# Kernel optimization log

Measured on AMD Instinct MI355X. Metric: run time of the kernel, lower is better.

Reference implementation:

```python
import jax, jax.numpy as jnp
from jax import lax
import numpy as np

KS = 8        # window size
SS = 4        # shift size = KS // 2
HEADS = 4


def _l2n(t, axis):
    # torch F.normalize: x / clamp(||x||_2, min=eps)
    return t / jnp.maximum(jnp.linalg.norm(t, axis=axis, keepdims=True), 1e-12)


def _to_windows(t, heads, ks):
    # 'b (head c) (h kh) (w kw) -> b head (h w) (kh kw) c'
    b, hc, H, W = t.shape
    c = hc // heads
    hW, wW = H // ks, W // ks
    t = t.reshape(b, heads, c, hW, ks, wW, ks)
    t = t.transpose(0, 1, 3, 5, 4, 6, 2)  # b,h,hW,wW,kh,kw,c
    return t.reshape(b, heads, hW * wW, ks * ks, c)


def _from_windows(t, hW, wW, ks):
    # 'b head (h w) (kh kw) c -> b (head c) (h kh) (w kw)'
    b, heads, nW, kk, c = t.shape
    t = t.reshape(b, heads, hW, wW, ks, ks, c)
    t = t.transpose(0, 1, 6, 2, 4, 3, 5)  # b,h,c,hW,kh,wW,kw
    return t.reshape(b, heads * c, hW * ks, wW * ks)


def _talk_conv(attn, w, hW, wW):
    # Conv3d(heads->heads, kernel (3,3,1), padding same) over the (hW, wW, K)
    # grid; kernel size 1 on K means an independent 2D conv per K slot, so we
    # fold K into the batch dim and run a single 2D conv.
    b, heads, nW, a1, a2 = attn.shape
    K = a1 * a2
    t = attn.reshape(b, heads, hW, wW, K).transpose(0, 4, 1, 2, 3)
    t = t.reshape(b * K, heads, hW, wW)
    t = lax.conv_general_dilated(t, w, (1, 1), 'SAME',
                                 dimension_numbers=('NCHW', 'OIHW', 'NCHW'))
    t = t.reshape(b, K, heads, hW, wW).transpose(0, 2, 3, 4, 1)
    return t.reshape(b, heads, nW, a1, a2)


def _shift_mask(H, W, ks, ss):
    # Swin-style shifted-window mask; pure numpy constant (shapes are static).
    img = np.zeros((H, W), np.float32)
    cnt = 0
    for hs in (slice(0, -ks), slice(-ks, -ss), slice(-ss, None)):
        for ws in (slice(0, -ks), slice(-ks, -ss), slice(-ss, None)):
            img[hs, ws] = cnt
            cnt += 1
    win = img.reshape(H // ks, ks, W // ks, ks).transpose(0, 2, 1, 3).reshape(-1, ks * ks)
    diff = win[:, None, :] - win[:, :, None]
    return jnp.asarray(np.where(diff != 0, -100.0, 0.0).astype(np.float32))


def _forward(x, w_quz, w_kv, temperature, r_talking, g_talking,
             b_talking_w, l_talking_w, dw_u_w, project_w, project_out_w,
             sca_w, sca_b):
    b, c, H, W = x.shape
    hW, wW = H // KS, W // KS
    quz = jnp.einsum('oc,bchw->bohw', w_quz, x)
    q, u, z = jnp.split(quz, 3, axis=1)
    kv = jnp.einsum('oc,bchw->bohw', w_kv, x)
    k, v = jnp.split(kv, 2, axis=1)
    # shift = True
    q, k, v = (jnp.roll(t, (-SS, -SS), axis=(-1, -2)) for t in (q, k, v))
    q, k, v = (_to_windows(t, HEADS, KS) for t in (q, k, v))  # b,h,nW,kk,c
    qb, ql, qg, qr = jnp.split(q, 4, axis=-1)
    kb, kl, kg, kr = jnp.split(k, 4, axis=-1)
    vb, vl, vg, vr = jnp.split(v, 4, axis=-1)
    qb, kb = _l2n(qb, -1), _l2n(kb, -1)
    ql, kl = _l2n(ql, -2), _l2n(kl, -2)
    qg, kg = _l2n(qg, -3), _l2n(kg, -3)
    qr, kr = _l2n(qr, -3), _l2n(kr, -3)
    # 4 branches (n=window index, i/j=position-in-window, c/d=per-branch chan)
    attn_b = jnp.einsum('bhnic,bhnjc->bhnij', qb, kb) * temperature[0]
    attn_l = jnp.einsum('bhnic,bhnid->bhncd', ql, kl) * temperature[1]
    attn_g = jnp.einsum('bhnic,bhnid->bhicd', qg, kg) * temperature[2]
    attn_r = jnp.einsum('bhnic,bhnjc->bhcij', qr, kr) * temperature[3]
    # talking heads
    attn_b = _talk_conv(attn_b, b_talking_w, hW, wW)
    attn_l = _talk_conv(attn_l, l_talking_w, hW, wW)
    attn_g = jnp.einsum('hklt,bhkcd->btlcd', g_talking, attn_g)
    attn_r = jnp.einsum('hcdt,bhcij->btdij', r_talking, attn_r)
    # shifted-window mask on the brightness branch
    attn_b = attn_b + _shift_mask(H, W, KS, SS)[None, None]
    attn_b, attn_l, attn_g, attn_r = (jax.nn.softmax(t, axis=-1)
                                      for t in (attn_b, attn_l, attn_g, attn_r))
    # outputs, all arranged to (b,h,n,i,c) before un-windowing
    out_b = jnp.einsum('bhnij,bhnjc->bhnic', attn_b, vb)
    out_l = jnp.einsum('bhncd,bhnid->bhnic', attn_l, vl)
    out_g = jnp.einsum('bhicd,bhnid->bhnic', attn_g, vg)
    out_r = jnp.einsum('bhcij,bhnjc->bhnic', attn_r, vr)
    out = jnp.concatenate([_from_windows(t, hW, wW, KS)
                           for t in (out_b, out_l, out_g, out_r)], axis=1)
    out = jnp.roll(out, (SS, SS), axis=(-1, -2))
    # simplified channel attention (global avg pool + 1x1 conv with bias)
    s = jnp.mean(out, axis=(2, 3))
    s = jnp.einsum('oc,bc->bo', sca_w, s) + sca_b
    out = jnp.einsum('oc,bchw->bohw', project_w, out * s[:, :, None, None])
    dw = lax.conv_general_dilated(u, dw_u_w, (1, 1), 'SAME',
                                  feature_group_count=u.shape[1],
                                  dimension_numbers=('NCHW', 'OIHW', 'NCHW'))
    out = out + dw
    return jnp.einsum('oc,bchw->bohw', project_out_w, out * z)


def setup_inputs() -> dict:
    key = jax.random.key(0)
    ks = jax.random.split(key, 12)
    dim, h_dim = 64, 128
    cd = h_dim // HEADS // 4
    b, H, W = 4, 192, 192
    r = lambda i, shp, s: jax.random.normal(ks[i], shp, jnp.float32) * s
    return {
        'x': jax.random.normal(ks[0], (b, dim, H, W), jnp.float32),
        'w_quz': r(1, (3 * h_dim, dim), 0.1),
        'w_kv': r(2, (2 * h_dim, dim), 0.1),
        'temperature': jnp.ones((4, HEADS, 1, 1, 1), jnp.float32),
        'r_talking': r(3, (HEADS, cd, cd, HEADS), 0.2),
        'g_talking': r(4, (HEADS, KS * KS, KS * KS, HEADS), 0.05),
        'b_talking_w': r(5, (HEADS, HEADS, 3, 3), 0.2),
        'l_talking_w': r(6, (HEADS, HEADS, 3, 3), 0.2),
        'dw_u_w': r(7, (h_dim, 1, 3, 3), 0.2),
        'project_w': r(8, (h_dim, h_dim), 0.08),
        'project_out_w': r(9, (dim, h_dim), 0.08),
        'sca_w': r(10, (h_dim, h_dim), 0.08),
        'sca_b': jnp.zeros((h_dim,), jnp.float32),
    }


def reference(x, w_quz, w_kv, temperature, r_talking, g_talking,
              b_talking_w, l_talking_w, dw_u_w, project_w, project_out_w,
              sca_w, sca_b):
    return _forward(x, w_quz, w_kv, temperature, r_talking, g_talking,
                    b_talking_w, l_talking_w, dw_u_w, project_w,
                    project_out_w, sca_w, sca_b)
```

## Files before the change

### kernel.cpp

```cpp
#include <hip/hip_runtime.h>
#include <hip/hip_fp16.h>
#include <cstdint>
#include <cstddef>

#define BB   4
#define CIN  64
#define HD   128
#define NH   4
#define CHW  32
#define CB   8
#define IMG  192
#define SSH  4
#define NWS  24
#define NWIN 576
#define KK   64
#define HWP  (IMG*IMG)

static const size_t NQK16  = (size_t)NH*NWIN*KK*16;
static const size_t NV32   = (size_t)NH*NWIN*KK*CHW;
static const size_t NGR    = (size_t)NH*KK*NWIN*CB;
static const size_t NSP    = (size_t)HD*HWP;
static const size_t NATTNL = (size_t)NH*NWIN*64;
static const size_t NATTNG = (size_t)NH*KK*64;
static const size_t NATTNR = (size_t)NH*CB*KK*KK;
static const size_t NPART  = (size_t)8*NATTNR;

__device__ inline float wave_max(float v){
  #pragma unroll
  for (int s=1;s<64;s<<=1) v = fmaxf(v, __shfl_xor(v, s));
  return v;
}
__device__ inline float wave_sum(float v){
  #pragma unroll
  for (int s=1;s<64;s<<=1) v += __shfl_xor(v, s);
  return v;
}
__device__ inline float g8_max(float v){
  v = fmaxf(v, __shfl_xor(v,1)); v = fmaxf(v, __shfl_xor(v,2)); v = fmaxf(v, __shfl_xor(v,4));
  return v;
}
__device__ inline float g8_sum(float v){
  v += __shfl_xor(v,1); v += __shfl_xor(v,2); v += __shfl_xor(v,4);
  return v;
}
__device__ inline int regionc(int y){ return (y < IMG-8) ? 0 : ((y < IMG-4) ? 1 : 2); }

__device__ inline size_t widx(int h,int n,int i,int c){
  return (((size_t)h*NWIN + n)*KK + i)*CHW + c;
}
__device__ inline size_t widx16(int h,int n,int i,int c){
  return (((size_t)h*NWIN + n)*KK + i)*16 + c;
}
__device__ inline size_t gidx(int h,int i,int n,int c){
  return (((size_t)(h*KK + i))*NWIN + n)*CB + c;
}
__device__ inline size_t ridx(int h,int c,int n,int i){
  return (((size_t)(h*CB + c))*NWIN + n)*KK + i;
}
__device__ inline size_t bidx(int n,int i,int j,int h){
  return ((((size_t)n*KK + i)*KK + j)*NH) + h;
}

__global__ __launch_bounds__(256) void k1_proj(
    const float* __restrict__ x, const float* __restrict__ wquz, const float* __restrict__ wkv,
    float* __restrict__ qw, float* __restrict__ kw, __half* __restrict__ vw,
    float* __restrict__ qg, float* __restrict__ kg,
    float* __restrict__ qr, float* __restrict__ kr,
    float* __restrict__ u, float* __restrict__ zbuf, int bsel)
{
  __shared__ float xs[64][20];
  __shared__ float tb[128][17];
  int blk = blockIdx.x;
  int xc = blk % 12, y = blk / 12;
  int x0 = xc*16;
  int t = threadIdx.x;
  {
    int c = t >> 2, p4 = (t & 3)*4;
    float4 v = *(const float4*)&x[((size_t)(bsel*CIN+c)*IMG + y)*IMG + x0 + p4];
    *(float4*)&xs[c][p4] = v;
  }
  int py  = (y + IMG - SSH) % IMG;
  int kh  = py & 7, hwq = py >> 3;
  int wwA = ((x0 - SSH + IMG) % IMG) >> 3;
  int wwB = x0 >> 3;
  int wwC = (x0 + 8) >> 3;
  int pnA = hwq*NWS + wwA, pnB = hwq*NWS + wwB, pnC = hwq*NWS + wwC;
  int piA = kh*8 + 4, piB = kh*8, piC = kh*8;
  #define PN_(p) ((p)<4 ? pnA : ((p)<12 ? pnB : pnC))
  #define PI_(p) ((p)<4 ? (piA+(p)) : ((p)<12 ? (piB+(p)-4) : (piC+(p)-12)))
  __syncthreads();

  int o;
  if (t < 64)       o = (t>>4)*32 + (t&15);
  else if (t < 96)  o = ((t-64)>>3)*32 + 16 + (t&7);
  else if (t < 128) o = ((t-96)>>3)*32 + 24 + (t&7);
  else              o = t;

  {
    const float* wr = wquz + (size_t)o*CIN;
    float acc[16];
    #pragma unroll
    for (int p = 0; p < 16; ++p) acc[p] = 0.f;
    for (int cc = 0; cc < 64; cc += 4){
      float4 w4 = *(const float4*)(wr + cc);
      #pragma unroll
      for (int p = 0; p < 16; ++p){
        acc[p] += w4.x * xs[cc  ][p];
        acc[p] += w4.y * xs[cc+1][p];
        acc[p] += w4.z * xs[cc+2][p];
        acc[p] += w4.w * xs[cc+3][p];
      }
    }
    if (t < 64){
      int h = t >> 4, c = t & 15;
      #pragma unroll
      for (int p = 0; p < 16; ++p) qw[widx16(h,PN_(p),PI_(p),c)] = acc[p];
    } else if (t < 96){
      int h = (t-64) >> 3, cg = t & 7;
      #pragma unroll
      for (int p = 0; p < 16; ++p) qg[gidx(h,PI_(p),PN_(p),cg)] = acc[p];
    } else if (t < 128){
      int h = (t-96) >> 3, cr = t & 7;
      *(float4*)&qr[ridx(h,cr,pnA,piA)]   = make_float4(acc[0],acc[1],acc[2],acc[3]);
      *(float4*)&qr[ridx(h,cr,pnB,piB)]   = make_float4(acc[4],acc[5],acc[6],acc[7]);
      *(float4*)&qr[ridx(h,cr,pnB,piB+4)] = make_float4(acc[8],acc[9],acc[10],acc[11]);
      *(float4*)&qr[ridx(h,cr,pnC,piC)]   = make_float4(acc[12],acc[13],acc[14],acc[15]);
    } else {
      int ch = o - 128;
      #pragma unroll
      for (int p = 0; p < 16; ++p) tb[ch][p] = acc[p];
    }
  }
  __syncthreads();
  {
    int px = t & 15, chg = t >> 4;
    size_t ub = (size_t)y*IMG + x0 + px;
    #pragma unroll
    for (int cc = 0; cc < 8; ++cc){
      int ch = chg*8 + cc;
      u[(size_t)ch*HWP + ub] = tb[ch][px];
    }
  }

  {
    const float* wr = wkv + (size_t)o*CIN;
    float acc[16];
    #pragma unroll
    for (int p = 0; p < 16; ++p) acc[p] = 0.f;
    for (int cc = 0; cc < 64; cc += 4){
      float4 w4 = *(const float4*)(wr + cc);
      #pragma unroll
      for (int p = 0; p < 16; ++p){
        acc[p] += w4.x * xs[cc  ][p];
        acc[p] += w4.y * xs[cc+1][p];
        acc[p] += w4.z * xs[cc+2][p];
        acc[p] += w4.w * xs[cc+3][p];
      }
    }
    if (t < 64){
      int h = t >> 4, c = t & 15;
      #pragma unroll
      for (int p = 0; p < 16; ++p) kw[widx16(h,PN_(p),PI_(p),c)] = acc[p];
    } else if (t < 96){
      int h = (t-64) >> 3, cg = t & 7;
      #pragma unroll
      for (int p = 0; p < 16; ++p) kg[gidx(h,PI_(p),PN_(p),cg)] = acc[p];
    } else if (t < 128){
      int h = (t-96) >> 3, cr = t & 7;
      *(float4*)&kr[ridx(h,cr,pnA,piA)]   = make_float4(acc[0],acc[1],acc[2],acc[3]);
      *(float4*)&kr[ridx(h,cr,pnB,piB)]   = make_float4(acc[4],acc[5],acc[6],acc[7]);
      *(float4*)&kr[ridx(h,cr,pnB,piB+4)] = make_float4(acc[8],acc[9],acc[10],acc[11]);
      *(float4*)&kr[ridx(h,cr,pnC,piC)]   = make_float4(acc[12],acc[13],acc[14],acc[15]);
    } else {
      int oc = o - 128; int h = oc >> 5, c = oc & 31;
      #pragma unroll
      for (int p = 0; p < 16; ++p) vw[widx(h,PN_(p),PI_(p),c)] = __float2half(acc[p]);
    }
  }

  __syncthreads();
  {
    int zr = t >> 1, ph = t & 1;
    const float* wr = wquz + (size_t)(256 + zr)*CIN;
    int pb = ph*8;
    float acc[8];
    #pragma unroll
    for (int p = 0; p < 8; ++p) acc[p] = 0.f;
    for (int cc = 0; cc < 64; cc += 4){
      float4 w4 = *(const float4*)(wr + cc);
      #pragma unroll
      for (int p = 0; p < 8; ++p){
        acc[p] += w4.x * xs[cc  ][pb+p];
        acc[p] += w4.y * xs[cc+1][pb+p];
        acc[p] += w4.z * xs[cc+2][pb+p];
        acc[p] += w4.w * xs[cc+3][pb+p];
      }
    }
    #pragma unroll
    for (int p = 0; p < 8; ++p) tb[zr][pb+p] = acc[p];
  }
  __syncthreads();
  {
    int px = t & 15, chg = t >> 4;
    size_t zb = (size_t)y*IMG + x0 + px;
    #pragma unroll
    for (int cc = 0; cc < 8; ++cc){
      int ch = chg*8 + cc;
      zbuf[(size_t)ch*HWP + zb] = tb[ch][px];
    }
  }
  #undef PN_
  #undef PI_
}

__global__ __launch_bounds__(256) void kA(
    const float* __restrict__ qw, const float* __restrict__ kw,
    const float* __restrict__ qg, const float* __restrict__ kg,
    const float* __restrict__ qr, const float* __restrict__ kr,
    const float* __restrict__ temp,
    __half* __restrict__ attnB, float* __restrict__ attnL,
    float* __restrict__ attnG, float* __restrict__ part,
    float* __restrict__ invqr, float* __restrict__ invkr)
{
  __shared__ __align__(16) char smem[36864];
  int blk = blockIdx.x;
  int t = threadIdx.x;

  if (blk < 576){
    float (*qs)[64][9] = (float(*)[64][9])smem;
    int j = t >> 2, h = t & 3;
    int n = blk;
    size_t base = widx16(h,n,j,0);
    float q8[CB], k8[CB];
    float sq = 0.f, sk2 = 0.f;
    #pragma unroll
    for (int c = 0; c < CB; ++c){
      q8[c] = qw[base+c]; sq += q8[c]*q8[c];
      k8[c] = kw[base+c]; sk2 += k8[c]*k8[c];
    }
    float invq = 1.f/fmaxf(sqrtf(sq),1e-12f), invk = 1.f/fmaxf(sqrtf(sk2),1e-12f);
    #pragma unroll
    for (int c = 0; c < CB; ++c){ qs[h][j][c] = q8[c]*invq; k8[c] *= invk; }
    __syncthreads();
    float tmp = temp[h];
    __half* ob = attnB + bidx(n,0,0,0);
    for (int i = 0; i < KK; ++i){
      float a = 0.f;
      #pragma unroll
      for (int c = 0; c < CB; ++c) a += qs[h][i][c]*k8[c];
      ob[(size_t)i*256 + t] = __float2half(a * tmp);
    }
  } else if (blk < 1152){
    int b2 = blk - 576;
    float (*qs)[64][8] = (float(*)[64][8])smem;
    float (*ks)[64][8] = (float(*)[64][8])(smem + 8192);
    float (*invqA)[8] = (float(*)[8])(smem + 16384);
    float (*invkA)[8] = (float(*)[8])(smem + 16384 + 128);
    int wv = t >> 6, tl = t & 63;
    int gid = b2*4 + wv;
    int n = gid % NWIN, h = gid / NWIN;
    size_t base = widx16(h,n,tl,8);
    #pragma unroll
    for (int c = 0; c < CB; ++c){ qs[wv][tl][c] = qw[base+c]; ks[wv][tl][c] = kw[base+c]; }
    __syncthreads();
    int c8 = tl & 7, ig = tl >> 3;
    float sq = 0.f, sk2 = 0.f;
    for (int i = ig; i < KK; i += 8){
      float a = qs[wv][i][c8]; sq += a*a;
      float b = ks[wv][i][c8]; sk2 += b*b;
    }
    #pragma unroll
    for (int m = 8; m < 64; m <<= 1){ sq += __shfl_xor(sq,m); sk2 += __shfl_xor(sk2,m); }
    if (tl < 8){ invqA[wv][tl] = 1.f/fmaxf(sqrtf(sq),1e-12f); invkA[wv][tl] = 1.f/fmaxf(sqrtf(sk2),1e-12f); }
    __syncthreads();
    int c = tl >> 3, d = tl & 7;
    float a = 0.f;
    for (int i = 0; i < KK; ++i) a += qs[wv][i][c]*ks[wv][i][d];
    attnL[(size_t)gid*64 + tl] = a * invqA[wv][c] * invkA[wv][d] * temp[NH + h];
  } else if (blk < 1408){
    int b2 = blk - 1152;
    int i = b2 & 63, h = b2 >> 6;
    float* sq = (float*)smem;
    float* sk = sq + 512;
    float (*redA)[64] = (float(*)[64])(smem + 4096);
    float (*redQ)[64] = (float(*)[64])(smem + 4096 + 1024);
    float (*redK)[64] = (float(*)[64])(smem + 4096 + 2048);
    size_t base = ((size_t)(h*KK+i))*NWIN*CB;
    int np = t >> 6, cd = t & 63, c = cd >> 3, d = cd & 7;
    float a = 0.f, qs2 = 0.f, ks2 = 0.f;
    for (int n0 = 0; n0 < NWIN; n0 += 64){
      __syncthreads();
      for (int idx = t; idx < 512; idx += 256){
        sq[idx] = qg[base + (size_t)n0*CB + idx];
        sk[idx] = kg[base + (size_t)n0*CB + idx];
      }
      __syncthreads();
      for (int nn = np; nn < 64; nn += 4){
        float qv = sq[nn*8+c], kv = sk[nn*8+d];
        a += qv*kv; qs2 += qv*qv; ks2 += kv*kv;
      }
    }
    __syncthreads();
    redA[np][cd] = a; redQ[np][cd] = qs2; redK[np][cd] = ks2;
    __syncthreads();
    if (t < 64){
      float at = redA[0][t]+redA[1][t]+redA[2][t]+redA[3][t];
      float qt = redQ[0][t]+redQ[1][t]+redQ[2][t]+redQ[3][t];
      float kt = redK[0][t]+redK[1][t]+redK[2][t]+redK[3][t];
      at *= (1.f/fmaxf(sqrtf(qt),1e-12f)) * (1.f/fmaxf(sqrtf(kt),1e-12f)) * temp[2*NH + h];
      attnG[(size_t)(h*KK+i)*64 + t] = at;
    }
  } else if (blk < 1664){
    int b2 = blk - 1408;
    int chunk = b2 >> 5, hc = b2 & 31;
    int n0 = chunk*72;
    float* sq = (float*)smem;
    float* sk = sq + 72*64;
    size_t base = (size_t)hc*NWIN*KK + (size_t)n0*KK;
    for (int idx = t; idx < 72*64/4; idx += 256){
      *(float4*)&sq[idx*4] = *(const float4*)&qr[base + (size_t)idx*4];
      *(float4*)&sk[idx*4] = *(const float4*)&kr[base + (size_t)idx*4];
    }
    __syncthreads();
    int j = t & 63, ig = t >> 6;
    float acc[16];
    #pragma unroll
    for (int p = 0; p < 16; ++p) acc[p] = 0.f;
    for (int nn = 0; nn < 72; ++nn){
      float kv = sk[nn*64+j];
      #pragma unroll
      for (int p = 0; p < 16; ++p) acc[p] += sq[nn*64 + ig*16 + p]*kv;
    }
    float* ob = part + (size_t)b2*4096;
    #pragma unroll
    for (int p = 0; p < 16; ++p) ob[(size_t)(ig*16+p)*64 + j] = acc[p];
  } else {
    int hc = blk - 1664;
    float (*rq)[64] = (float(*)[64])smem;
    float (*rk)[64] = (float(*)[64])(smem + 1024);
    size_t base = (size_t)hc*NWIN*KK;
    int i = t & 63, ng = t >> 6;
    float sq = 0.f, sk2 = 0.f;
    for (int n = ng; n < NWIN; n += 4){
      float a = qr[base + (size_t)n*KK + i]; sq  += a*a;
      float b = kr[base + (size_t)n*KK + i]; sk2 += b*b;
    }
    rq[ng][i] = sq; rk[ng][i] = sk2;
    __syncthreads();
    if (t < 64){
      float s = rq[0][t]+rq[1][t]+rq[2][t]+rq[3][t];
      invqr[hc*KK + t] = 1.f/fmaxf(sqrtf(s),1e-12f);
    } else if (t < 128){
      int i2 = t - 64;
      float s = rk[0][i2]+rk[1][i2]+rk[2][i2]+rk[3][i2];
      invkr[hc*KK + i2] = 1.f/fmaxf(sqrtf(s),1e-12f);
    }
  }
}

__global__ __launch_bounds__(256) void kB(
    const __half* __restrict__ attnB, const float* __restrict__ btw,
    const __half* __restrict__ vw, float* __restrict__ outa,
    const float* __restrict__ attnL, const float* __restrict__ ltw,
    const float* __restrict__ attnG, const float* __restrict__ gtalk,
    float* __restrict__ attnGp,
    const float* __restrict__ part, const float* __restrict__ invqr,
    const float* __restrict__ invkr, const float* __restrict__ temp,
    float* __restrict__ attnR,
    const float* __restrict__ u, const float* __restrict__ dww,
    float* __restrict__ dwu)
{
  __shared__ __align__(16) char smem[12800];
  int blk = blockIdx.x;
  int t = threadIdx.x;

  if (blk < 9216){
    float (*pbuf)[4][66] = (float(*)[4][66])smem;
    float (*vv)[8][66]   = (float(*)[8][66])(smem + 4224);
    int ig = blk / NWIN, n = blk % NWIN;
    int i0 = ig*4;
    int hw = n / NWS, ww = n % NWS;
    int w = t >> 6, l = t & 63;
    {
      uint4 pk = *(const uint4*)(vw + widx(w, n, l, 0));
      __half2 v01 = *reinterpret_cast<__half2*>(&pk.x);
      __half2 v23 = *reinterpret_cast<__half2*>(&pk.y);
      __half2 v45 = *reinterpret_cast<__half2*>(&pk.z);
      __half2 v67 = *reinterpret_cast<__half2*>(&pk.w);
      float2 f01 = __half22float2(v01), f23 = __half22float2(v23);
      float2 f45 = __half22float2(v45), f67 = __half22float2(v67);
      vv[w][0][l] = f01.x; vv[w][1][l] = f01.y; vv[w][2][l] = f23.x; vv[w][3][l] = f23.y;
      vv[w][4][l] = f45.x; vv[w][5][l] = f45.y; vv[w][6][l] = f67.x; vv[w][7][l] = f67.y;
    }
    int i = i0 + w;
    float a0 = 0.f, a1 = 0.f, a2 = 0.f, a3 = 0.f;
    #pragma unroll
    for (int nb = 0; nb < 9; ++nb){
      const int dy = nb/3 - 1, dx = nb%3 - 1;
      int hw2 = hw + dy, ww2 = ww + dx;
      if (hw2 >= 0 && hw2 < NWS && ww2 >= 0 && ww2 < NWS){
        int n2 = hw2*NWS + ww2;
        const uint2* pb = (const uint2*)(attnB + bidx(n2, i, 0, 0));
        uint2 pk = pb[l];
        __half2 p01 = *reinterpret_cast<__half2*>(&pk.x);
        __half2 p23 = *reinterpret_cast<__half2*>(&pk.y);
        float2 f01 = __half22float2(p01);
        float2 f23 = __half22float2(p23);
        a0 += btw[0*36 + 0*9 + nb]*f01.x + btw[0*36 + 1*9 + nb]*f01.y
            + btw[0*36 + 2*9 + nb]*f23.x + btw[0*36 + 3*9 + nb]*f23.y;
        a1 += btw[1*36 + 0*9 + nb]*f01.x + btw[1*36 + 1*9 + nb]*f01.y
            + btw[1*36 + 2*9 + nb]*f23.x + btw[1*36 + 3*9 + nb]*f23.y;
        a2 += btw[2*36 + 0*9 + nb]*f01.x + btw[2*36 + 1*9 + nb]*f01.y
            + btw[2*36 + 2*9 + nb]*f23.x + btw[2*36 + 3*9 + nb]*f23.y;
        a3 += btw[3*36 + 0*9 + nb]*f01.x + btw[3*36 + 1*9 + nb]*f01.y
            + btw[3*36 + 2*9 + nb]*f23.x + btw[3*36 + 3*9 + nb]*f23.y;
      }
    }
    int kh = i >> 3, kwd = i & 7;
    int cntI = regionc(hw*8 + kh)*3 + regionc(ww*8 + kwd);
    int cntJ = regionc(hw*8 + (l>>3))*3 + regionc(ww*8 + (l&7));
    float mval = (cntI != cntJ) ? -100.f : 0.f;
    a0 += mval; a1 += mval; a2 += mval; a3 += mval;
    {
      float m0 = wave_max(a0); float e0 = __expf(a0 - m0); pbuf[0][w][l] = e0 / wave_sum(e0);
      float m1 = wave_max(a1); float e1 = __expf(a1 - m1); pbuf[1][w][l] = e1 / wave_sum(e1);
      float m2 = wave_max(a2); float e2 = __expf(a2 - m2); pbuf[2][w][l] = e2 / wave_sum(e2);
      float m3 = wave_max(a3); float e3 = __expf(a3 - m3); pbuf[3][w][l] = e3 / wave_sum(e3);
    }
    __syncthreads();
    {
      int i2 = l >> 4, c = (l >> 1) & 7, jq = l & 1;
      const float* pr = &pbuf[w][i2][jq*32];
      const float* vr = &vv[w][c][jq*32];
      float s = 0.f;
      #pragma unroll
      for (int q = 0; q < 32; ++q) s += pr[q] * vr[q];
      s += __shfl_xor(s, 1);
      if (jq == 0){
        int ii = i0 + i2;
        int khh = ii >> 3, kww = ii & 7;
        int Y = (hw*8 + khh + SSH) % IMG;
        int X = (ww*8 + kww + SSH) % IMG;
        outa[((size_t)(w*CB + c)*HWP) + (size_t)Y*IMG + X] = s;
      }
    }
  } else if (blk < 9792){
    int n = blk - 9216;
    int hw = n/NWS, ww = n%NWS;
    float (*rows)[9][64] = (float(*)[9][64])smem;
    float* wt = (float*)(smem + 9216);
    float (*P)[8][8] = (float(*)[8][8])(smem + 9792);
    if (t < NH*NH*9) wt[t] = ltw[t];
    for (int l = t; l < NH*9*64; l += 256){
      int h = l/(9*64); int nb = (l/64)%9; int cd = l & 63;
      int dy = nb/3-1, dx = nb%3-1; int hw2 = hw+dy, ww2 = ww+dx;
      float v = 0.f;
      if (hw2>=0 && hw2<NWS && ww2>=0 && ww2<NWS)
        v = attnL[((size_t)h*NWIN + hw2*NWS + ww2)*64 + cd];
      rows[h][nb][cd] = v;
    }
    __syncthreads();
    int tt = t >> 6; int cd = t & 63; int c = cd >> 3, d = cd & 7;
    float a = 0.f;
    #pragma unroll
    for (int h = 0; h < NH; ++h)
      #pragma unroll
      for (int nb = 0; nb < 9; ++nb)
        a += wt[(tt*NH + h)*9 + nb] * rows[h][nb][cd];
    float m = g8_max(a);
    float e = __expf(a - m);
    P[tt][c][d] = e / g8_sum(e);
    __syncthreads();
    int i = t & 63;
    size_t vbase = widx(tt, n, i, 8);
    float vl[CB];
    #pragma unroll
    for (int d2 = 0; d2 < CB; ++d2) vl[d2] = __half2float(vw[vbase + d2]);
    int kh = i>>3, kwd = i&7;
    int Y = (hw*8+kh+SSH)%IMG, X = (ww*8+kwd+SSH)%IMG;
    #pragma unroll
    for (int c2 = 0; c2 < CB; ++c2){
      float o = 0.f;
      #pragma unroll
      for (int d2 = 0; d2 < CB; ++d2) o += P[tt][c2][d2]*vl[d2];
      outa[((size_t)(32 + tt*CB + c2)*IMG + Y)*IMG + X] = o;
    }
  } else if (blk < 9856){
    int bb = blk - 9792;
    int w = t >> 6, cd = t & 63;
    int idx = bb*4 + w;
    int l = idx & 63, t2 = idx >> 6;
    float a = 0.f;
    for (int h = 0; h < NH; ++h)
      for (int k = 0; k < KK; ++k)
        a += gtalk[((size_t)(h*KK + k)*KK + l)*NH + t2] * attnG[((size_t)h*KK + k)*64 + cd];
    float m = g8_max(a);
    float e = __expf(a - m);
    attnGp[((size_t)t2*KK + l)*64 + cd] = e / g8_sum(e);
  } else if (blk < 10368){
    int e = (blk - 9856)*256 + t;
    float s = 0.f;
    #pragma unroll
    for (int ch = 0; ch < 8; ++ch) s += part[(size_t)ch*NATTNR + e];
    int hc = e >> 12, ij = e & 4095, i = ij >> 6, j = ij & 63;
    attnR[e] = s * invqr[hc*64+i] * invkr[hc*64+j] * temp[3*NH + (hc>>3)];
  } else {
    int bb = blk - 10368;
    int ch = bb / 48; int y0 = (bb % 48) * 4;
    float (*rows)[192] = (float(*)[192])smem;
    for (int idx = t; idx < 6*48; idx += 256){
      int r = idx / 48, px4 = (idx % 48)*4;
      int yy = y0 - 1 + r;
      float4 v = {0.f,0.f,0.f,0.f};
      if (yy >= 0 && yy < IMG) v = *(const float4*)&u[(size_t)ch*HWP + (size_t)yy*IMG + px4];
      rows[r][px4] = v.x; rows[r][px4+1] = v.y; rows[r][px4+2] = v.z; rows[r][px4+3] = v.w;
    }
    float kw9[9];
    #pragma unroll
    for (int q = 0; q < 9; ++q) kw9[q] = dww[ch*9 + q];
    __syncthreads();
    int r = t >> 6, lane = t & 63;
    for (int kx = 0; kx < 3; ++kx){
      int px = lane + kx*64;
      float s = 0.f;
      #pragma unroll
      for (int dy = 0; dy < 3; ++dy){
        #pragma unroll
        for (int dx = -1; dx <= 1; ++dx){
          int xx = px + dx;
          if (xx >= 0 && xx < IMG) s += kw9[dy*3 + dx + 1] * rows[r+dy][xx];
        }
      }
      dwu[(size_t)ch*HWP + (size_t)(y0+r)*IMG + px] = s;
    }
  }
}

__global__ __launch_bounds__(256) void kC(
    const float* __restrict__ attnGp, const __half* __restrict__ vw,
    float* __restrict__ outa,
    const float* __restrict__ attnR, const float* __restrict__ rtalk,
    float* __restrict__ attnRp)
{
  __shared__ __align__(16) char smem[16512];
  int blk = blockIdx.x;
  int t = threadIdx.x;

  if (blk < 2304){
    float* P = (float*)smem;
    int n = blk % NWIN; int t2 = blk / NWIN;
    for (int l = t; l < KK*64; l += 256) P[l] = attnGp[(size_t)t2*KK*64 + l];
    __syncthreads();
    int i = t >> 2; int c0 = (t & 3)*2;
    size_t vbase = widx(t2, n, i, 16);
    float vg[8];
    #pragma unroll
    for (int d = 0; d < 8; ++d) vg[d] = __half2float(vw[vbase + d]);
    int hw = n/NWS, ww = n%NWS; int kh = i>>3, kwd = i&7;
    int Y = (hw*8+kh+SSH)%IMG, X = (ww*8+kwd+SSH)%IMG;
    for (int c = c0; c < c0+2; ++c){
      float o = 0.f;
      #pragma unroll
      for (int d = 0; d < 8; ++d) o += P[(i*8 + c)*8 + d]*vg[d];
      outa[((size_t)(64 + t2*CB + c)*IMG + Y)*IMG + X] = o;
    }
  } else {
    int bb = blk - 2304;
    int d = bb % CB; int t2 = bb / CB;
    float (*S)[64] = (float(*)[64])smem;
    float* wr2 = (float*)(smem + 16384);
    if (t < 32){ int h = t >> 3, c = t & 7; wr2[t] = rtalk[((size_t)(h*CB + c)*CB + d)*NH + t2]; }
    __syncthreads();
    int j = t & 63; int ig = t >> 6;
    float acc[16];
    #pragma unroll
    for (int p = 0; p < 16; ++p) acc[p] = 0.f;
    for (int hc = 0; hc < 32; ++hc){
      float w = wr2[hc];
      const float* Ar = attnR + (size_t)hc*KK*KK;
      #pragma unroll
      for (int p = 0; p < 16; ++p) acc[p] += w * Ar[(size_t)(ig*16+p)*KK + j];
    }
    #pragma unroll
    for (int p = 0; p < 16; ++p) S[ig*16+p][j] = acc[p];
    __syncthreads();
    for (int r = ig; r < 64; r += 4){
      float a = S[r][j];
      float m = wave_max(a);
      float e = __expf(a - m);
      attnRp[(((size_t)t2*CB + d)*KK + r)*KK + j] = e / wave_sum(e);
    }
  }
}

__global__ __launch_bounds__(256) void k7c(
    const float* __restrict__ attnRp, const __half* __restrict__ vw, float* __restrict__ outa)
{
  int n = blockIdx.x % NWIN; int t2 = blockIdx.x / NWIN;
  __shared__ float vr[KK][CB];
  int t = threadIdx.x;
  for (int l = t; l < KK*CB; l += 256){
    int j = l >> 3, c = l & 7;
    vr[j][c] = __half2float(vw[widx(t2, n, j, 24 + c)]);
  }
  __syncthreads();
  int i = t & 63; int cg = t >> 6;
  int hw = n/NWS, ww = n%NWS; int kh = i>>3, kwd = i&7;
  int Y = (hw*8+kh+SSH)%IMG, X = (ww*8+kwd+SSH)%IMG;
  for (int c = cg*2; c < cg*2+2; ++c){
    const float* Pr = attnRp + (((size_t)t2*CB + c)*KK + i)*KK;
    float o = 0.f;
    for (int j = 0; j < KK; ++j) o += Pr[j]*vr[j][c];
    outa[((size_t)(96 + t2*CB + c)*IMG + Y)*IMG + X] = o;
  }
}

__global__ __launch_bounds__(256) void k8_mean(const float* __restrict__ outa, float* __restrict__ meanb){
  int ch = blockIdx.x;
  const float4* p = (const float4*)(outa + (size_t)ch*HWP);
  float s = 0.f;
  for (int l = threadIdx.x; l < HWP/4; l += 256){
    float4 v = p[l]; s += v.x+v.y+v.z+v.w;
  }
  __shared__ float red[256];
  red[threadIdx.x] = s; __syncthreads();
  for (int k = 128; k > 0; k >>= 1){
    if (threadIdx.x < k) red[threadIdx.x] += red[threadIdx.x + k];
    __syncthreads();
  }
  if (threadIdx.x == 0) meanb[ch] = red[0] / (float)HWP;
}

#define PADX 68
__global__ __launch_bounds__(256) void k9a(
    const float* __restrict__ outa, const float* __restrict__ meanb,
    const float* __restrict__ scaw, const float* __restrict__ scab,
    const float* __restrict__ projw, const float* __restrict__ dwu,
    const float* __restrict__ zbuf, float* __restrict__ out2z)
{
  __shared__ float WT[128][128];
  __shared__ float xsv[128][PADX];
  __shared__ float sv[128];
  int t = threadIdx.x;
  if (t < 128){
    float s = scab[t];
    const float* srow = scaw + (size_t)t*HD;
    for (int c = 0; c < HD; c += 4){
      float4 w = *(const float4*)&srow[c];
      float4 mm = *(const float4*)&meanb[c];
      s += w.x*mm.x + w.y*mm.y + w.z*mm.z + w.w*mm.w;
    }
    sv[t] = s;
  }
  for (int idx = t; idx < 4096; idx += 256){
    int o = idx & 127; int c4 = (idx >> 7) * 4;
    float4 w = *(const float4*)&projw[(size_t)o*HD + c4];
    WT[c4][o] = w.x; WT[c4+1][o] = w.y; WT[c4+2][o] = w.z; WT[c4+3][o] = w.w;
  }
  int px4 = (t & 15) * 4; int og8 = (t >> 4) * 8;
  for (int tile = 0; tile < 2; ++tile){
    int tid = blockIdx.x * 2 + tile;
    int y = tid / 3, x0 = (tid % 3) * 64;
    size_t sb = (size_t)y*IMG + x0;
    __syncthreads();
    for (int idx = t; idx < 2048; idx += 256){
      int c = idx >> 4; int p4 = (idx & 15) * 4;
      float4 v = *(const float4*)&outa[(size_t)c*HWP + sb + p4];
      float s = sv[c];
      xsv[c][p4] = v.x*s; xsv[c][p4+1] = v.y*s; xsv[c][p4+2] = v.z*s; xsv[c][p4+3] = v.w*s;
    }
    __syncthreads();
    float acc[8][4];
    #pragma unroll
    for (int a = 0; a < 8; ++a){ acc[a][0]=0.f; acc[a][1]=0.f; acc[a][2]=0.f; acc[a][3]=0.f; }
    for (int c = 0; c < 128; ++c){
      float4 xv = *(const float4*)&xsv[c][px4];
      float4 wA = *(const float4*)&WT[c][og8];
      float4 wB = *(const float4*)&WT[c][og8+4];
      float w8[8] = {wA.x,wA.y,wA.z,wA.w,wB.x,wB.y,wB.z,wB.w};
      #pragma unroll
      for (int a = 0; a < 8; ++a){
        acc[a][0] += w8[a]*xv.x; acc[a][1] += w8[a]*xv.y;
        acc[a][2] += w8[a]*xv.z; acc[a][3] += w8[a]*xv.w;
      }
    }
    #pragma unroll
    for (int oo = 0; oo < 8; ++oo){
      int o = og8 + oo;
      size_t off = (size_t)o*HWP + sb + px4;
      float4 d = *(const float4*)&dwu[off];
      float4 z = *(const float4*)&zbuf[off];
      float4 r;
      r.x = (acc[oo][0]+d.x)*z.x; r.y = (acc[oo][1]+d.y)*z.y;
      r.z = (acc[oo][2]+d.z)*z.z; r.w = (acc[oo][3]+d.w)*z.w;
      *(float4*)&out2z[off] = r;
    }
  }
}

__global__ __launch_bounds__(256) void k9b(
    const float* __restrict__ out2z, const float* __restrict__ projow,
    float* __restrict__ dout, int bsel)
{
  __shared__ float WT2[128][64];
  __shared__ float xsv[128][PADX];
  int t = threadIdx.x;
  for (int idx = t; idx < 2048; idx += 256){
    int o = idx & 63; int c4 = (idx >> 6) * 4;
    float4 w = *(const float4*)&projow[(size_t)o*HD + c4];
    WT2[c4][o] = w.x; WT2[c4+1][o] = w.y; WT2[c4+2][o] = w.z; WT2[c4+3][o] = w.w;
  }
  int px4 = (t & 15) * 4; int og4 = (t >> 4) * 4;
  for (int tile = 0; tile < 2; ++tile){
    int tid = blockIdx.x * 2 + tile;
    int y = tid / 3, x0 = (tid % 3) * 64;
    size_t sb = (size_t)y*IMG + x0;
    __syncthreads();
    for (int idx = t; idx < 2048; idx += 256){
      int c = idx >> 4; int p4 = (idx & 15) * 4;
      float4 v = *(const float4*)&out2z[(size_t)c*HWP + sb + p4];
      xsv[c][p4] = v.x; xsv[c][p4+1] = v.y; xsv[c][p4+2] = v.z; xsv[c][p4+3] = v.w;
    }
    __syncthreads();
    float acc[4][4];
    #pragma unroll
    for (int a = 0; a < 4; ++a){ acc[a][0]=0.f; acc[a][1]=0.f; acc[a][2]=0.f; acc[a][3]=0.f; }
    for (int c = 0; c < 128; ++c){
      float4 xv = *(const float4*)&xsv[c][px4];
      float4 w4 = *(const float4*)&WT2[c][og4];
      float w4a[4] = {w4.x,w4.y,w4.z,w4.w};
      #pragma unroll
      for (int a = 0; a < 4; ++a){
        acc[a][0] += w4a[a]*xv.x; acc[a][1] += w4a[a]*xv.y;
        acc[a][2] += w4a[a]*xv.z; acc[a][3] += w4a[a]*xv.w;
      }
    }
    #pragma unroll
    for (int oo = 0; oo < 4; ++oo){
      int o = og4 + oo;
      float4 r; r.x = acc[oo][0]; r.y = acc[oo][1]; r.z = acc[oo][2]; r.w = acc[oo][3];
      *(float4*)&dout[(size_t)(bsel*CIN + o)*HWP + sb + px4] = r;
    }
  }
}

extern "C" void kernel_launch(void* const* d_in, const int* in_sizes, int n_in,
                              void* d_out, int out_size, void* d_ws, size_t ws_size,
                              hipStream_t stream)
{
  const float* x     = (const float*)d_in[0];
  const float* wquz  = (const float*)d_in[1];
  const float* wkv   = (const float*)d_in[2];
  const float* temp  = (const float*)d_in[3];
  const float* rtalk = (const float*)d_in[4];
  const float* gtalk = (const float*)d_in[5];
  const float* btw   = (const float*)d_in[6];
  const float* ltw   = (const float*)d_in[7];
  const float* dww   = (const float*)d_in[8];
  const float* projw = (const float*)d_in[9];
  const float* projow= (const float*)d_in[10];
  const float* scaw  = (const float*)d_in[11];
  const float* scab  = (const float*)d_in[12];
  float* dout = (float*)d_out;

  float* ws = (float*)d_ws;
  float* qw    = ws;
  float* kw    = qw + NQK16;
  float* vwf   = kw + NQK16;
  __half* vwh  = (__half*)vwf;
  float* qg    = vwf + NV32;
  float* kg    = qg + NGR;
  float* qr    = kg + NGR;
  float* kr    = qr + NGR;
  float* u     = kr + NGR;
  float* zbuf  = u + NSP;
  float* outa  = zbuf + NSP;
  float* attnBf= outa + NSP;
  __half* attnBh = (__half*)attnBf;
  float* attnL = attnBf + NSP;
  float* attnG = attnL + NATTNL;
  float* attnGp= attnG + NATTNG;
  float* part  = attnGp + NATTNG;
  float* attnR = part + NPART;
  float* attnRp= attnR + NATTNR;
  float* invqr = attnRp + NATTNR;
  float* invkr = invqr + 2048;
  float* meanb = invkr + 2048;
  float* dwu   = qw;
  float* out2z = attnBf;

  for (int b = 0; b < BB; ++b){
    k1_proj<<<IMG*12, 256, 0, stream>>>(x, wquz, wkv, qw, kw, vwh, qg, kg, qr, kr, u, zbuf, b);

    kA<<<1696, 256, 0, stream>>>(qw, kw, qg, kg, qr, kr, temp,
                                 attnBh, attnL, attnG, part, invqr, invkr);

    kB<<<16512, 256, 0, stream>>>(attnBh, btw, vwh, outa, attnL, ltw,
                                  attnG, gtalk, attnGp, part, invqr, invkr, temp, attnR,
                                  u, dww, dwu);

    kC<<<2336, 256, 0, stream>>>(attnGp, vwh, outa, attnR, rtalk, attnRp);

    k7c<<<NH*NWIN, 256, 0, stream>>>(attnRp, vwh, outa);

    k8_mean<<<HD, 256, 0, stream>>>(outa, meanb);

    k9a<<<288, 256, 0, stream>>>(outa, meanb, scaw, scab, projw, dwu, zbuf, out2z);
    k9b<<<288, 256, 0, stream>>>(out2z, projow, dout, b);
  }
}
```

Baseline: 1.212 ms.

## Batch multiple images per kernel launch using per-batch workspace slices

Replaces the per-image launch loop with launches that cover up to four images at once. Each block derives its batch index from blockIdx and offsets every workspace pointer by a per-batch stride, provided the workspace is large enough. This cuts launch count and fills the GPU better for small kernels like k8_mean and k9. The cost is a larger workspace footprint and extra index arithmetic per block, and the code falls back to one image per launch if the workspace is too small.

```diff
diff --git a/kernel.cpp b/kernel.cpp
--- a/kernel.cpp
+++ b/kernel.cpp
@@ -25,6 +25,14 @@
 static const size_t NATTNR = (size_t)NH*CB*KK*KK;
 static const size_t NPART  = (size_t)8*NATTNR;
 
+#define PB_K1  (IMG*12)
+#define PB_KA  1696
+#define PB_KB  16512
+#define PB_KC  2336
+#define PB_K7C 2304
+#define PB_K8  128
+#define PB_K9  288
+
 __device__ inline float wave_max(float v){
   #pragma unroll
   for (int s=1;s<64;s<<=1) v = fmaxf(v, __shfl_xor(v, s));
@@ -66,11 +74,17 @@
     float* __restrict__ qw, float* __restrict__ kw, __half* __restrict__ vw,
     float* __restrict__ qg, float* __restrict__ kg,
     float* __restrict__ qr, float* __restrict__ kr,
-    float* __restrict__ u, float* __restrict__ zbuf, int bsel)
+    float* __restrict__ u, float* __restrict__ zbuf, int b0, size_t bstr)
 {
+  int lb = blockIdx.x / PB_K1;
+  int blk = blockIdx.x - lb*PB_K1;
+  int bsel = b0 + lb;
+  size_t off = (size_t)lb*bstr;
+  qw += off; kw += off; qg += off; kg += off; qr += off; kr += off;
+  u += off; zbuf += off; vw += off*2;
+
   __shared__ float xs[64][20];
   __shared__ float tb[128][17];
-  int blk = blockIdx.x;
   int xc = blk % 12, y = blk / 12;
   int x0 = xc*16;
   int t = threadIdx.x;
@@ -220,10 +234,16 @@
     const float* __restrict__ temp,
     __half* __restrict__ attnB, float* __restrict__ attnL,
     float* __restrict__ attnG, float* __restrict__ part,
-    float* __restrict__ invqr, float* __restrict__ invkr)
+    float* __restrict__ invqr, float* __restrict__ invkr, size_t bstr)
 {
+  int lb = blockIdx.x / PB_KA;
+  int blk = blockIdx.x - lb*PB_KA;
+  size_t off = (size_t)lb*bstr;
+  qw += off; kw += off; qg += off; kg += off; qr += off; kr += off;
+  attnL += off; attnG += off; part += off; invqr += off; invkr += off;
+  attnB += off*2;
+
   __shared__ __align__(16) char smem[36864];
-  int blk = blockIdx.x;
   int t = threadIdx.x;
 
   if (blk < 576){
@@ -368,10 +388,16 @@
     const float* __restrict__ invkr, const float* __restrict__ temp,
     float* __restrict__ attnR,
     const float* __restrict__ u, const float* __restrict__ dww,
-    float* __restrict__ dwu)
+    float* __restrict__ dwu, size_t bstr)
 {
+  int lb = blockIdx.x / PB_KB;
+  int blk = blockIdx.x - lb*PB_KB;
+  size_t off = (size_t)lb*bstr;
+  attnB += off*2; vw += off*2;
+  outa += off; attnL += off; attnG += off; attnGp += off;
+  part += off; invqr += off; invkr += off; attnR += off; u += off; dwu += off;
+
   __shared__ __align__(16) char smem[12800];
-  int blk = blockIdx.x;
   int t = threadIdx.x;
 
   if (blk < 9216){
@@ -540,10 +566,14 @@
     const float* __restrict__ attnGp, const __half* __restrict__ vw,
     float* __restrict__ outa,
     const float* __restrict__ attnR, const float* __restrict__ rtalk,
-    float* __restrict__ attnRp)
+    float* __restrict__ attnRp, size_t bstr)
 {
+  int lb = blockIdx.x / PB_KC;
+  int blk = blockIdx.x - lb*PB_KC;
+  size_t off = (size_t)lb*bstr;
+  attnGp += off; outa += off; attnR += off; attnRp += off; vw += off*2;
+
   __shared__ __align__(16) char smem[16512];
-  int blk = blockIdx.x;
   int t = threadIdx.x;
 
   if (blk < 2304){
@@ -594,9 +624,15 @@
 }
 
 __global__ __launch_bounds__(256) void k7c(
-    const float* __restrict__ attnRp, const __half* __restrict__ vw, float* __restrict__ outa)
+    const float* __restrict__ attnRp, const __half* __restrict__ vw, float* __restrict__ outa,
+    size_t bstr)
 {
-  int n = blockIdx.x % NWIN; int t2 = blockIdx.x / NWIN;
+  int lb = blockIdx.x / PB_K7C;
+  int blk = blockIdx.x - lb*PB_K7C;
+  size_t off = (size_t)lb*bstr;
+  attnRp += off; outa += off; vw += off*2;
+
+  int n = blk % NWIN; int t2 = blk / NWIN;
   __shared__ float vr[KK][CB];
   int t = threadIdx.x;
   for (int l = t; l < KK*CB; l += 256){
@@ -615,8 +651,14 @@
   }
 }
 
-__global__ __launch_bounds__(256) void k8_mean(const float* __restrict__ outa, float* __restrict__ meanb){
-  int ch = blockIdx.x;
+__global__ __launch_bounds__(256) void k8_mean(const float* __restrict__ outa, float* __restrict__ meanb,
+                                               size_t bstr)
+{
+  int lb = blockIdx.x / PB_K8;
+  int ch = blockIdx.x - lb*PB_K8;
+  size_t off = (size_t)lb*bstr;
+  outa += off; meanb += off;
+
   const float4* p = (const float4*)(outa + (size_t)ch*HWP);
   float s = 0.f;
   for (int l = threadIdx.x; l < HWP/4; l += 256){
@@ -636,8 +678,13 @@
     const float* __restrict__ outa, const float* __restrict__ meanb,
     const float* __restrict__ scaw, const float* __restrict__ scab,
     const float* __restrict__ projw, const float* __restrict__ dwu,
-    const float* __restrict__ zbuf, float* __restrict__ out2z)
+    const float* __restrict__ zbuf, float* __restrict__ out2z, size_t bstr)
 {
+  int lb = blockIdx.x / PB_K9;
+  int blk = blockIdx.x - lb*PB_K9;
+  size_t off = (size_t)lb*bstr;
+  outa += off; meanb += off; dwu += off; zbuf += off; out2z += off;
+
   __shared__ float WT[128][128];
   __shared__ float xsv[128][PADX];
   __shared__ float sv[128];
@@ -659,7 +706,7 @@
   }
   int px4 = (t & 15) * 4; int og8 = (t >> 4) * 8;
   for (int tile = 0; tile < 2; ++tile){
-    int tid = blockIdx.x * 2 + tile;
+    int tid = blk * 2 + tile;
     int y = tid / 3, x0 = (tid % 3) * 64;
     size_t sb = (size_t)y*IMG + x0;
     __syncthreads();
@@ -687,21 +734,26 @@
     #pragma unroll
     for (int oo = 0; oo < 8; ++oo){
       int o = og8 + oo;
-      size_t off = (size_t)o*HWP + sb + px4;
-      float4 d = *(const float4*)&dwu[off];
-      float4 z = *(const float4*)&zbuf[off];
+      size_t off2 = (size_t)o*HWP + sb + px4;
+      float4 d = *(const float4*)&dwu[off2];
+      float4 z = *(const float4*)&zbuf[off2];
       float4 r;
       r.x = (acc[oo][0]+d.x)*z.x; r.y = (acc[oo][1]+d.y)*z.y;
       r.z = (acc[oo][2]+d.z)*z.z; r.w = (acc[oo][3]+d.w)*z.w;
-      *(float4*)&out2z[off] = r;
+      *(float4*)&out2z[off2] = r;
     }
   }
 }
 
 __global__ __launch_bounds__(256) void k9b(
     const float* __restrict__ out2z, const float* __restrict__ projow,
-    float* __restrict__ dout, int bsel)
+    float* __restrict__ dout, int b0, size_t bstr)
 {
+  int lb = blockIdx.x / PB_K9;
+  int blk = blockIdx.x - lb*PB_K9;
+  int bsel = b0 + lb;
+  out2z += (size_t)lb*bstr;
+
   __shared__ float WT2[128][64];
   __shared__ float xsv[128][PADX];
   int t = threadIdx.x;
@@ -712,7 +764,7 @@
   }
   int px4 = (t & 15) * 4; int og4 = (t >> 4) * 4;
   for (int tile = 0; tile < 2; ++tile){
-    int tid = blockIdx.x * 2 + tile;
+    int tid = blk * 2 + tile;
     int y = tid / 3, x0 = (tid % 3) * 64;
     size_t sb = (size_t)y*IMG + x0;
     __syncthreads();
@@ -764,48 +816,75 @@
   float* dout = (float*)d_out;
 
   float* ws = (float*)d_ws;
-  float* qw    = ws;
-  float* kw    = qw + NQK16;
-  float* vwf   = kw + NQK16;
-  __half* vwh  = (__half*)vwf;
-  float* qg    = vwf + NV32;
-  float* kg    = qg + NGR;
-  float* qr    = kg + NGR;
-  float* kr    = qr + NGR;
-  float* u     = kr + NGR;
-  float* zbuf  = u + NSP;
-  float* outa  = zbuf + NSP;
-  float* attnBf= outa + NSP;
-  __half* attnBh = (__half*)attnBf;
-  float* attnL = attnBf + NSP;
-  float* attnG = attnL + NATTNL;
-  float* attnGp= attnG + NATTNG;
-  float* part  = attnGp + NATTNG;
-  float* attnR = part + NPART;
-  float* attnRp= attnR + NATTNR;
-  float* invqr = attnRp + NATTNR;
-  float* invkr = invqr + 2048;
-  float* meanb = invkr + 2048;
+  size_t oqw    = 0;
+  size_t okw    = oqw + NQK16;
+  size_t ovw    = okw + NQK16;
+  size_t oqg    = ovw + NV32;
+  size_t okg    = oqg + NGR;
+  size_t oqr    = okg + NGR;
+  size_t okr    = oqr + NGR;
+  size_t ou     = okr + NGR;
+  size_t ozbuf  = ou + NSP;
+  size_t oouta  = ozbuf + NSP;
+  size_t oattnB = oouta + NSP;
+  size_t oattnL = oattnB + NSP;
+  size_t oattnG = oattnL + NATTNL;
+  size_t oattnGp= oattnG + NATTNG;
+  size_t opart  = oattnGp + NATTNG;
+  size_t oattnR = opart + NPART;
+  size_t oattnRp= oattnR + NATTNR;
+  size_t oinvqr = oattnRp + NATTNR;
+  size_t oinvkr = oinvqr + 2048;
+  size_t omeanb = oinvkr + 2048;
+  size_t bstr   = omeanb + 128;
+
+  int NB = 1;
+  if (ws_size >= 4*bstr*sizeof(float))      NB = 4;
+  else if (ws_size >= 2*bstr*sizeof(float)) NB = 2;
+
+  float* qw    = ws + oqw;
+  float* kw    = ws + okw;
+  __half* vwh  = (__half*)(ws + ovw);
+  float* qg    = ws + oqg;
+  float* kg    = ws + okg;
+  float* qr    = ws + oqr;
+  float* kr    = ws + okr;
+  float* u     = ws + ou;
+  float* zbuf  = ws + ozbuf;
+  float* outa  = ws + oouta;
+  __half* attnBh = (__half*)(ws + oattnB);
+  float* attnL = ws + oattnL;
+  float* attnG = ws + oattnG;
+  float* attnGp= ws + oattnGp;
+  float* part  = ws + opart;
+  float* attnR = ws + oattnR;
+  float* attnRp= ws + oattnRp;
+  float* invqr = ws + oinvqr;
+  float* invkr = ws + oinvkr;
+  float* meanb = ws + omeanb;
   float* dwu   = qw;
-  float* out2z = attnBf;
-
-  for (int b = 0; b < BB; ++b){
-    k1_proj<<<IMG*12, 256, 0, stream>>>(x, wquz, wkv, qw, kw, vwh, qg, kg, qr, kr, u, zbuf, b);
-
-    kA<<<1696, 256, 0, stream>>>(qw, kw, qg, kg, qr, kr, temp,
-                                 attnBh, attnL, attnG, part, invqr, invkr);
-
-    kB<<<16512, 256, 0, stream>>>(attnBh, btw, vwh, outa, attnL, ltw,
-                                  attnG, gtalk, attnGp, part, invqr, invkr, temp, attnR,
-                                  u, dww, dwu);
-
-    kC<<<2336, 256, 0, stream>>>(attnGp, vwh, outa, attnR, rtalk, attnRp);
-
-    k7c<<<NH*NWIN, 256, 0, stream>>>(attnRp, vwh, outa);
-
-    k8_mean<<<HD, 256, 0, stream>>>(outa, meanb);
-
-    k9a<<<288, 256, 0, stream>>>(outa, meanb, scaw, scab, projw, dwu, zbuf, out2z);
-    k9b<<<288, 256, 0, stream>>>(out2z, projow, dout, b);
-  }
-}
+  float* out2z = ws + oattnB;
+
+  for (int b0 = 0; b0 < BB; b0 += NB){
+    int nb = (BB - b0 < NB) ? (BB - b0) : NB;
+
+    k1_proj<<<PB_K1*nb, 256, 0, stream>>>(x, wquz, wkv, qw, kw, vwh, qg, kg, qr, kr,
+                                          u, zbuf, b0, bstr);
+
+    kA<<<PB_KA*nb, 256, 0, stream>>>(qw, kw, qg, kg, qr, kr, temp,
+                                     attnBh, attnL, attnG, part, invqr, invkr, bstr);
+
+    kB<<<PB_KB*nb, 256, 0, stream>>>(attnBh, btw, vwh, outa, attnL, ltw,
+                                     attnG, gtalk, attnGp, part, invqr, invkr, temp, attnR,
+                                     u, dww, dwu, bstr);
+
+    kC<<<PB_KC*nb, 256, 0, stream>>>(attnGp, vwh, outa, attnR, rtalk, attnRp, bstr);
+
+    k7c<<<PB_K7C*nb, 256, 0, stream>>>(attnRp, vwh, outa, bstr);
+
+    k8_mean<<<PB_K8*nb, 256, 0, stream>>>(outa, meanb, bstr);
+
+    k9a<<<PB_K9*nb, 256, 0, stream>>>(outa, meanb, scaw, scab, projw, dwu, zbuf, out2z, bstr);
+    k9b<<<PB_K9*nb, 256, 0, stream>>>(out2z, projow, dout, b0, bstr);
+  }
+}
```

Result: no change. 1.205 ms (-0.5%).
